# Optimization experiments

Hardware: AMD Instinct MI355X
Metric: run time of the kernel (lower is better)

## Reference

```python
import jax, jax.numpy as jnp
import numpy as np
from jax import lax

TAU = 2.0
V_TH = 1.0
ALPHA = 4.0   # spikingjelly surrogate.Sigmoid default
BN_EPS = 1e-5
HEADS = 8


def lif(x):
    """Multi-step LIF neuron (tau=2, v_reset=0, hard reset, detach_reset).
    x: [T, ...] -> spikes [T, ...]. Forward is Heaviside; sigmoid surrogate
    is wired in via straight-through for the bwd variant."""
    def step(v, xt):
        v = v + (xt - v) / TAU                      # charge
        sg = jax.nn.sigmoid(ALPHA * (v - V_TH))     # surrogate
        hard = (v >= V_TH).astype(x.dtype)
        spike = sg + lax.stop_gradient(hard - sg)   # fwd: hard, bwd: sigmoid'
        v = v * (1.0 - lax.stop_gradient(spike))    # detached hard reset to 0
        return v, spike
    _, s = lax.scan(step, jnp.zeros_like(x[0]), x)
    return s


def conv1x1_bn(x, w, g, b, m, var, bias=None):
    # x: [N, C, H, W]; 1x1 conv == channel matmul, then eval-mode BN
    y = jnp.einsum('nchw,dc->ndhw', x, w)
    if bias is not None:
        y = y + bias[None, :, None, None]
    scale = g / jnp.sqrt(var + BN_EPS)
    shift = b - m * scale
    return y * scale[None, :, None, None] + shift[None, :, None, None]


def to_heads(x, T, B, C, H, W):
    # [T,B,C,H,W] -> [T,B,heads,N,hd]
    N = H * W
    hd = C // HEADS
    x = x.reshape(T, B, C, N).transpose(0, 1, 3, 2)          # [T,B,N,C]
    return x.reshape(T, B, N, HEADS, hd).transpose(0, 1, 3, 2, 4)


def _forward(x, q_w, q_bn_g, q_bn_b, q_bn_m, q_bn_v,
             k_w, k_bn_g, k_bn_b, k_bn_m, k_bn_v,
             v_w, v_bn_g, v_bn_b, v_bn_m, v_bn_v,
             out_w, out_b, out_bn_g, out_bn_b, out_bn_m, out_bn_v):
    T, B, C, H, W = x.shape
    N = H * W
    identity = x

    xs = lif(x)                                  # shortcut_lif
    x_qkv = xs.reshape(T * B, C, H, W)

    q = lif(conv1x1_bn(x_qkv, q_w, q_bn_g, q_bn_b, q_bn_m, q_bn_v).reshape(T, B, C, H, W))
    k = lif(conv1x1_bn(x_qkv, k_w, k_bn_g, k_bn_b, k_bn_m, k_bn_v).reshape(T, B, C, H, W))
    v = lif(conv1x1_bn(x_qkv, v_w, v_bn_g, v_bn_b, v_bn_m, v_bn_v).reshape(T, B, C, H, W))

    qh = to_heads(q, T, B, C, H, W)              # [T,B,h,N,hd]
    kh = to_heads(k, T, B, C, H, W)
    vh = to_heads(v, T, B, C, H, W)

    kv = jnp.sum(kh * vh, axis=-2, keepdims=True)   # [T,B,h,1,hd]
    kv = lif(kv)                                    # talking_heads_proj_lif
    y = qh * kv                                     # [T,B,h,N,hd]

    # [T,B,h,N,hd] -> transpose(3,4) -> [T,B,h,hd,N] -> [T,B,C,H,W]
    y = y.transpose(0, 1, 2, 4, 3).reshape(T, B, C, H, W)
    y = conv1x1_bn(y.reshape(T * B, C, H, W), out_w, out_bn_g, out_bn_b,
                   out_bn_m, out_bn_v, bias=out_b).reshape(T, B, C, H, W)
    return y + identity, vh


def setup_inputs() -> dict:
    key = jax.random.key(0)
    ks = jax.random.split(key, 6)
    T, B, C, H, W = 4, 32, 512, 14, 14
    inp = {
        'x': jax.random.normal(ks[0], (T, B, C, H, W), dtype=jnp.float32),
        'q_w': jax.random.normal(ks[1], (C, C), dtype=jnp.float32) * 0.05,
        'k_w': jax.random.normal(ks[2], (C, C), dtype=jnp.float32) * 0.05,
        'v_w': jax.random.normal(ks[3], (C, C), dtype=jnp.float32) * 0.05,
        'out_w': jax.random.normal(ks[4], (C, C), dtype=jnp.float32) * 0.05,
        'out_b': jnp.zeros((C,), dtype=jnp.float32),
    }
    for p in ('q', 'k', 'v', 'out'):
        inp[f'{p}_bn_g'] = jnp.ones((C,), dtype=jnp.float32)
        inp[f'{p}_bn_b'] = jnp.zeros((C,), dtype=jnp.float32)
        inp[f'{p}_bn_m'] = jnp.zeros((C,), dtype=jnp.float32)
        inp[f'{p}_bn_v'] = jnp.ones((C,), dtype=jnp.float32)
    return inp


def reference(x, q_w, q_bn_g, q_bn_b, q_bn_m, q_bn_v,
              k_w, k_bn_g, k_bn_b, k_bn_m, k_bn_v,
              v_w, v_bn_g, v_bn_b, v_bn_m, v_bn_v,
              out_w, out_b, out_bn_g, out_bn_b, out_bn_m, out_bn_v):
    return _forward(x, q_w, q_bn_g, q_bn_b, q_bn_m, q_bn_v,
                    k_w, k_bn_g, k_bn_b, k_bn_m, k_bn_v,
                    v_w, v_bn_g, v_bn_b, v_bn_m, v_bn_v,
                    out_w, out_b, out_bn_g, out_bn_b, out_bn_m, out_bn_v)
```

## Files before the change

### kernel.cpp

```cpp
#include <hip/hip_runtime.h>
#include <math.h>

#define T_   4
#define B_   32
#define C_   512
#define N_   196
#define TB_  128
#define M_   25088
#define BNP_ 6272
#define OUT1_ 12845056

typedef unsigned short ushort_t;
typedef __attribute__((ext_vector_type(8)))  __bf16 bf16x8;
typedef __attribute__((ext_vector_type(16))) float  f32x16;

__device__ __forceinline__ ushort_t f2bf(float f) {
    unsigned int u = __float_as_uint(f);
    u = u + 0x7FFFu + ((u >> 16) & 1u);
    return (ushort_t)(u >> 16);
}
__device__ __forceinline__ float bf2f(ushort_t h) {
    return __uint_as_float(((unsigned int)h) << 16);
}

#define GL2LDS(gp, lp) \
    __builtin_amdgcn_global_load_lds((const __attribute__((address_space(1))) void*)(gp), \
                                     (__attribute__((address_space(3))) void*)(lp), 16, 0, 0)

__global__ void bn_prep_kernel(
    const float* __restrict__ qg, const float* __restrict__ qb, const float* __restrict__ qm, const float* __restrict__ qv,
    const float* __restrict__ kg, const float* __restrict__ kb, const float* __restrict__ km, const float* __restrict__ kvr,
    const float* __restrict__ vg, const float* __restrict__ vb, const float* __restrict__ vm, const float* __restrict__ vv,
    const float* __restrict__ og, const float* __restrict__ ob, const float* __restrict__ om, const float* __restrict__ ov,
    const float* __restrict__ obias,
    float* __restrict__ scale_qkv, float* __restrict__ shift_qkv,
    float* __restrict__ scale_o,   float* __restrict__ shift_o)
{
    int i = blockIdx.x * 256 + threadIdx.x;
    if (i < 3 * C_) {
        int p = i >> 9, dl = i & 511;
        const float* g = (p == 0) ? qg : (p == 1) ? kg : vg;
        const float* b = (p == 0) ? qb : (p == 1) ? kb : vb;
        const float* m = (p == 0) ? qm : (p == 1) ? km : vm;
        const float* r = (p == 0) ? qv : (p == 1) ? kvr : vv;
        float sc = g[dl] / sqrtf(r[dl] + 1e-5f);
        scale_qkv[i] = sc;
        shift_qkv[i] = b[dl] - m[dl] * sc;
    }
    if (i < C_) {
        float sc = og[i] / sqrtf(ov[i] + 1e-5f);
        scale_o[i] = sc;
        shift_o[i] = ob[i] - om[i] * sc + obias[i] * sc;
    }
}

__global__ void split_kernel(const float* __restrict__ qw, const float* __restrict__ kw,
                             const float* __restrict__ vw, const float* __restrict__ ow,
                             ushort_t* __restrict__ wsplit, ushort_t* __restrict__ osplit)
{
    int i = blockIdx.x * 256 + threadIdx.x;
    int d = i >> 9, c = i & 511;
    const float* src = (d < 512) ? qw : (d < 1024) ? kw : vw;
    float wv = src[(d & 511) * 512 + c];
    ushort_t h = f2bf(wv);
    float r1 = wv - bf2f(h);
    ushort_t mm = f2bf(r1);
    float r2 = r1 - bf2f(mm);
    ushort_t l = f2bf(r2);
    wsplit[((size_t)d * 3 + 0) * 512 + c] = h;
    wsplit[((size_t)d * 3 + 1) * 512 + c] = mm;
    wsplit[((size_t)d * 3 + 2) * 512 + c] = l;
    if (d < 512)
        osplit[(size_t)d * 512 + c] = f2bf(ow[d * 512 + c]);
}

__global__ __launch_bounds__(256)
void lifx_kernel(const float* __restrict__ x, ushort_t* __restrict__ xs)
{
    __shared__ ushort_t tile[64 * 66];
    const int tid = threadIdx.x;
    const int b = blockIdx.z, c0 = blockIdx.y * 64, n0 = blockIdx.x * 64;
    const int j = tid & 63, w = tid >> 6;
    const bool nok = (n0 + j) < N_;
    float v[16];
#pragma unroll
    for (int r = 0; r < 16; ++r) v[r] = 0.f;
    for (int t = 0; t < T_; ++t) {
        const float* xb = x + ((size_t)((t * B_ + b) * C_ + c0)) * N_ + n0 + j;
#pragma unroll
        for (int r = 0; r < 16; ++r) {
            int i = w * 16 + r;
            float xv = nok ? xb[(size_t)i * N_] : 0.f;
            v[r] = v[r] + (xv - v[r]) * 0.5f;
            bool s = (v[r] >= 1.0f);
            tile[j * 66 + i] = s ? 0x3F80 : 0;
            if (s) v[r] = 0.f;
        }
        __syncthreads();
#pragma unroll
        for (int p = 0; p < 2; ++p) {
            int w2 = tid + p * 256;
            int jj = w2 >> 3, ck = w2 & 7;
            if (n0 + jj < N_) {
                const unsigned int* src = reinterpret_cast<const unsigned int*>(&tile[jj * 66 + ck * 8]);
                uint4 dv; dv.x = src[0]; dv.y = src[1]; dv.z = src[2]; dv.w = src[3];
                size_t mp = (size_t)(b * N_ + n0 + jj) * 4 + t;
                *reinterpret_cast<uint4*>(&xs[mp * 512 + c0 + ck * 8]) = dv;
            }
        }
        __syncthreads();
    }
}

__global__ __launch_bounds__(256, 2)
void qkv_gemm_lif(const ushort_t* __restrict__ W, const ushort_t* __restrict__ X,
                  const float* __restrict__ scale, const float* __restrict__ shift,
                  ushort_t* __restrict__ spk, float* __restrict__ out2)
{
    __shared__ ushort_t Xs[16 * 512];
    __shared__ ushort_t Ws[24 * 512];
    const int tid = threadIdx.x, wid = tid >> 6, lane = tid & 63;
    const int m0 = blockIdx.x * 256;
    const int d0 = blockIdx.y * 128;
    const int mw = (wid & 1) * 128, dw = (wid >> 1) * 64;
    const int row32 = lane & 31, khalf = lane >> 5;

    f32x16 acc[4][2] = {};

    for (int k0 = 0; k0 < 512; k0 += 32) {
        __syncthreads();
        for (int q = wid; q < 16; q += 4) {
            int mb = q >> 1, ks = q & 1;
            const ushort_t* g = X + (size_t)(m0 + mb * 32 + row32) * 512 + k0 + ks * 16 + khalf * 8;
            GL2LDS(g, &Xs[q * 512]);
        }
        for (int q = wid; q < 24; q += 4) {
            int s = q >> 3, rem = q & 7, db = rem >> 1, ks = rem & 1;
            const ushort_t* g = W + ((size_t)(d0 + db * 32 + row32) * 3 + s) * 512 + k0 + ks * 16 + khalf * 8;
            GL2LDS(g, &Ws[q * 512]);
        }
        __syncthreads();

#pragma unroll
        for (int ks = 0; ks < 2; ++ks) {
            bf16x8 xfr[4];
#pragma unroll
            for (int i = 0; i < 4; ++i)
                xfr[i] = *reinterpret_cast<const bf16x8*>(&Xs[(((mw >> 5) + i) * 2 + ks) * 512 + lane * 8]);
#pragma unroll
            for (int s = 0; s < 3; ++s)
#pragma unroll
                for (int j = 0; j < 2; ++j) {
                    bf16x8 wfr = *reinterpret_cast<const bf16x8*>(
                        &Ws[(s * 8 + ((dw >> 5) + j) * 2 + ks) * 512 + lane * 8]);
#pragma unroll
                    for (int i = 0; i < 4; ++i)
                        acc[i][j] = __builtin_amdgcn_mfma_f32_32x32x16_bf16(xfr[i], wfr, acc[i][j], 0, 0, 0);
                }
        }
    }

    const int p = d0 >> 9;
    const bool isV = (p == 2);
    ushort_t* plane = spk + (size_t)p * ((size_t)M_ * 512);
#pragma unroll
    for (int j = 0; j < 2; ++j) {
        int d = d0 + dw + j * 32 + row32;
        float sc = scale[d], sh = shift[d];
        int dl = d & 511;
        int h = dl >> 6, hd = dl & 63;
#pragma unroll
        for (int i = 0; i < 4; ++i) {
            int bnb = (m0 + mw + i * 32) >> 2;
            f32x16 a = acc[i][j];
#pragma unroll
            for (int g = 0; g < 4; ++g) {
                int bn = bnb + 2 * g + khalf;
                float p0 = fmaf(a[4 * g + 0], sc, sh);
                float p1 = fmaf(a[4 * g + 1], sc, sh);
                float p2 = fmaf(a[4 * g + 2], sc, sh);
                float p3 = fmaf(a[4 * g + 3], sc, sh);
                float v = p0 * 0.5f;
                bool s0 = (v >= 1.f); if (s0) v = 0.f;
                v = v + (p1 - v) * 0.5f;
                bool s1 = (v >= 1.f); if (s1) v = 0.f;
                v = v + (p2 - v) * 0.5f;
                bool s2 = (v >= 1.f); if (s2) v = 0.f;
                v = v + (p3 - v) * 0.5f;
                bool s3 = (v >= 1.f);
                ushort_t* b0 = plane + (size_t)bn * 512 + dl;
                b0[0]                      = s0 ? 0x3F80 : 0;
                b0[(size_t)BNP_ * 512]     = s1 ? 0x3F80 : 0;
                b0[(size_t)2 * BNP_ * 512] = s2 ? 0x3F80 : 0;
                b0[(size_t)3 * BNP_ * 512] = s3 ? 0x3F80 : 0;
                if (isV) {
                    int b = bn / N_, n = bn - b * N_;
                    float* o = out2 + (((size_t)b * 8 + h) * N_ + n) * 64 + hd;
                    o[0]                       = s0 ? 1.f : 0.f;
                    o[(size_t)1 * (OUT1_ / 4)] = s1 ? 1.f : 0.f;
                    o[(size_t)2 * (OUT1_ / 4)] = s2 ? 1.f : 0.f;
                    o[(size_t)3 * (OUT1_ / 4)] = s3 ? 1.f : 0.f;
                }
            }
        }
    }
}

__global__ void kv_part_kernel(const ushort_t* __restrict__ ks, const ushort_t* __restrict__ vs,
                               float* __restrict__ kvpart)
{
    int tb = blockIdx.x >> 1;
    int c  = (blockIdx.x & 1) * 256 + threadIdx.x;
    const ushort_t* kb = ks + (size_t)tb * N_ * 512 + c;
    const ushort_t* vb = vs + (size_t)tb * N_ * 512 + c;
    int cnt = 0;
    for (int n = 0; n < N_; ++n)
        cnt += (kb[(size_t)n * 512] & vb[(size_t)n * 512]) ? 1 : 0;
    kvpart[tb * 512 + c] = (float)cnt;
}

__global__ void kv_lif_kernel(const float* __restrict__ kvpart, ushort_t* __restrict__ kvs)
{
    int i = blockIdx.x * 256 + threadIdx.x;
    if (i >= B_ * C_) return;
    int b = i >> 9, c = i & 511;
    float v = 0.f;
#pragma unroll
    for (int t = 0; t < T_; ++t) {
        float y = kvpart[((t * B_ + b) << 9) + c];
        v = v + (y - v) * 0.5f;
        bool s = (v >= 1.f);
        kvs[((t * B_ + b) << 9) + c] = s ? 0x3F80 : 0;
        if (s) v = 0.f;
    }
}

__global__ void muly_kernel(const ushort_t* __restrict__ qs, const ushort_t* __restrict__ kvs,
                            ushort_t* __restrict__ y)
{
    int i = blockIdx.x * 256 + threadIdx.x;
    int m = i >> 6, cq = (i & 63) * 8;
    int tb = m / N_;
    uint4 q = *reinterpret_cast<const uint4*>(&qs[(size_t)m * 512 + cq]);
    uint4 k = *reinterpret_cast<const uint4*>(&kvs[(size_t)tb * 512 + cq]);
    uint4 o; o.x = q.x & k.x; o.y = q.y & k.y; o.z = q.z & k.z; o.w = q.w & k.w;
    *reinterpret_cast<uint4*>(&y[(size_t)m * 512 + cq]) = o;
}

__global__ __launch_bounds__(256)
void out_gemm(const ushort_t* __restrict__ A, const ushort_t* __restrict__ Bm,
              const float* __restrict__ scale, const float* __restrict__ shift,
              const float* __restrict__ xid, float* __restrict__ out)
{
    __shared__ ushort_t As[8 * 512];
    __shared__ ushort_t Bs[8 * 512];
    const int tid = threadIdx.x, wid = tid >> 6, lane = tid & 63;
    const int d0 = blockIdx.y * 128, m0 = blockIdx.x * 128;
    const int dw = (wid >> 1) * 64, mw = (wid & 1) * 64;
    const int row32 = lane & 31, khalf = lane >> 5;

    f32x16 acc[2][2] = {};

    for (int k0 = 0; k0 < 512; k0 += 32) {
        __syncthreads();
        for (int q = wid; q < 8; q += 4) {
            int db = q >> 1, ks = q & 1;
            const ushort_t* g = A + (size_t)(d0 + db * 32 + row32) * 512 + k0 + ks * 16 + khalf * 8;
            GL2LDS(g, &As[q * 512]);
        }
        for (int q = wid; q < 8; q += 4) {
            int mb = q >> 1, ks = q & 1;
            const ushort_t* g = Bm + (size_t)(m0 + mb * 32 + row32) * 512 + k0 + ks * 16 + khalf * 8;
            GL2LDS(g, &Bs[q * 512]);
        }
        __syncthreads();

#pragma unroll
        for (int ks = 0; ks < 2; ++ks) {
            bf16x8 afr[2];
#pragma unroll
            for (int i = 0; i < 2; ++i)
                afr[i] = *reinterpret_cast<const bf16x8*>(&As[(((dw >> 5) + i) * 2 + ks) * 512 + lane * 8]);
#pragma unroll
            for (int j = 0; j < 2; ++j) {
                bf16x8 bfr = *reinterpret_cast<const bf16x8*>(&Bs[(((mw >> 5) + j) * 2 + ks) * 512 + lane * 8]);
#pragma unroll
                for (int i = 0; i < 2; ++i)
                    acc[i][j] = __builtin_amdgcn_mfma_f32_32x32x16_bf16(afr[i], bfr, acc[i][j], 0, 0, 0);
            }
        }
    }

#pragma unroll
    for (int j = 0; j < 2; ++j) {
        int m = m0 + mw + j * 32 + row32;
        int tb = m / N_;
        int n  = m - tb * N_;
        size_t mbase = (size_t)tb * (C_ * N_) + n;
#pragma unroll
        for (int i = 0; i < 2; ++i) {
            int dbase = d0 + dw + i * 32 + 4 * khalf;
            f32x16 a = acc[i][j];
#pragma unroll
            for (int g = 0; g < 4; ++g) {
#pragma unroll
                for (int t = 0; t < 4; ++t) {
                    int d = dbase + t + 8 * g;
                    float val = fmaf(a[4 * g + t], scale[d], shift[d]);
                    size_t ad = mbase + (size_t)d * N_;
                    out[ad] = val + xid[ad];
                }
            }
        }
    }
}

extern "C" void kernel_launch(void* const* d_in, const int* in_sizes, int n_in,
                              void* d_out, int out_size, void* d_ws, size_t ws_size,
                              hipStream_t stream)
{
    const float* x    = (const float*)d_in[0];
    const float* q_w  = (const float*)d_in[1];
    const float* k_w  = (const float*)d_in[2];
    const float* v_w  = (const float*)d_in[3];
    const float* o_w  = (const float*)d_in[4];
    const float* o_b  = (const float*)d_in[5];
    const float* qg = (const float*)d_in[6],  *qb = (const float*)d_in[7],
               *qm = (const float*)d_in[8],  *qv = (const float*)d_in[9];
    const float* kg = (const float*)d_in[10], *kb = (const float*)d_in[11],
               *km = (const float*)d_in[12], *kv = (const float*)d_in[13];
    const float* vg = (const float*)d_in[14], *vb = (const float*)d_in[15],
               *vm = (const float*)d_in[16], *vv = (const float*)d_in[17];
    const float* og = (const float*)d_in[18], *ob = (const float*)d_in[19],
               *om = (const float*)d_in[20], *ov = (const float*)d_in[21];

    float* out1  = (float*)d_out;
    float* out2f = out1 + OUT1_;

    ushort_t* spk    = (ushort_t*)d_ws;
    ushort_t* xs     = spk + (size_t)3 * M_ * 512;
    ushort_t* wsplit = xs + (size_t)M_ * 512;
    ushort_t* osplit = wsplit + (size_t)1536 * 3 * 512;
    float*    kvpart = (float*)(osplit + (size_t)512 * 512);
    ushort_t* kvs    = (ushort_t*)(kvpart + TB_ * C_);
    float*    scq    = (float*)(kvs + TB_ * C_);
    float*    shq    = scq + 3 * C_;
    float*    sco    = shq + 3 * C_;
    float*    sho    = sco + C_;

    ushort_t* ksp = spk + (size_t)M_ * 512;
    ushort_t* vsp = spk + (size_t)2 * M_ * 512;

    bn_prep_kernel<<<8, 256, 0, stream>>>(qg, qb, qm, qv, kg, kb, km, kv,
                                          vg, vb, vm, vv, og, ob, om, ov, o_b,
                                          scq, shq, sco, sho);

    split_kernel<<<(1536 * 512) / 256, 256, 0, stream>>>(q_w, k_w, v_w, o_w, wsplit, osplit);

    lifx_kernel<<<dim3(4, 8, 32), 256, 0, stream>>>(x, xs);

    qkv_gemm_lif<<<dim3(98, 12), 256, 0, stream>>>(wsplit, xs, scq, shq, spk, out2f);

    kv_part_kernel<<<256, 256, 0, stream>>>(ksp, vsp, kvpart);

    kv_lif_kernel<<<64, 256, 0, stream>>>(kvpart, kvs);

    muly_kernel<<<(M_ * 64) / 256, 256, 0, stream>>>(spk, kvs, xs );

    out_gemm<<<dim3(196, 4), 256, 0, stream>>>(osplit, xs, sco, sho, x, out1);
}
```

Baseline: 450.8 us.

## Fuse prep kernels, drop third weight split, fuse mask into out GEMM, remap blocks

Merges the BN-prep and weight-split kernels into one launch and cuts the QKV weight split from three bf16 terms to two, reducing MFMA work and weight traffic by a third. The q·kv masking kernel is removed: out_gemm now ANDs q spikes with kv spikes while staging its B tile into LDS, so the intermediate y is never written or re-read. kv_part is split into four row chunks per channel and combined with atomicAdd, with the accumulator zeroed in the prep kernel. Both GEMMs switch to 1D grids with an XCD-aware swizzle for L2 locality. Dropping the third split term lowers precision of the pre-LIF activations, which may flip spikes near threshold.

```diff
diff --git a/kernel.cpp b/kernel.cpp
--- a/kernel.cpp
+++ b/kernel.cpp
@@ -27,16 +27,31 @@
     __builtin_amdgcn_global_load_lds((const __attribute__((address_space(1))) void*)(gp), \
                                      (__attribute__((address_space(3))) void*)(lp), 16, 0, 0)
 
-__global__ void bn_prep_kernel(
+__global__ void prep_kernel(
+    const float* __restrict__ qw, const float* __restrict__ kw,
+    const float* __restrict__ vw, const float* __restrict__ ow,
     const float* __restrict__ qg, const float* __restrict__ qb, const float* __restrict__ qm, const float* __restrict__ qv,
     const float* __restrict__ kg, const float* __restrict__ kb, const float* __restrict__ km, const float* __restrict__ kvr,
     const float* __restrict__ vg, const float* __restrict__ vb, const float* __restrict__ vm, const float* __restrict__ vv,
     const float* __restrict__ og, const float* __restrict__ ob, const float* __restrict__ om, const float* __restrict__ ov,
     const float* __restrict__ obias,
+    ushort_t* __restrict__ wsplit, ushort_t* __restrict__ osplit,
     float* __restrict__ scale_qkv, float* __restrict__ shift_qkv,
-    float* __restrict__ scale_o,   float* __restrict__ shift_o)
+    float* __restrict__ scale_o,   float* __restrict__ shift_o,
+    float* __restrict__ kvpart)
 {
     int i = blockIdx.x * 256 + threadIdx.x;
+    int d = i >> 9, c = i & 511;
+    const float* src = (d < 512) ? qw : (d < 1024) ? kw : vw;
+    float wv = src[(d & 511) * 512 + c];
+    ushort_t h = f2bf(wv);
+    float r1 = wv - bf2f(h);
+    ushort_t mm = f2bf(r1);
+    wsplit[((size_t)d * 2 + 0) * 512 + c] = h;
+    wsplit[((size_t)d * 2 + 1) * 512 + c] = mm;
+    if (d < 512)
+        osplit[(size_t)d * 512 + c] = f2bf(ow[d * 512 + c]);
+
     if (i < 3 * C_) {
         int p = i >> 9, dl = i & 511;
         const float* g = (p == 0) ? qg : (p == 1) ? kg : vg;
@@ -52,26 +67,7 @@
         scale_o[i] = sc;
         shift_o[i] = ob[i] - om[i] * sc + obias[i] * sc;
     }
-}
-
-__global__ void split_kernel(const float* __restrict__ qw, const float* __restrict__ kw,
-                             const float* __restrict__ vw, const float* __restrict__ ow,
-                             ushort_t* __restrict__ wsplit, ushort_t* __restrict__ osplit)
-{
-    int i = blockIdx.x * 256 + threadIdx.x;
-    int d = i >> 9, c = i & 511;
-    const float* src = (d < 512) ? qw : (d < 1024) ? kw : vw;
-    float wv = src[(d & 511) * 512 + c];
-    ushort_t h = f2bf(wv);
-    float r1 = wv - bf2f(h);
-    ushort_t mm = f2bf(r1);
-    float r2 = r1 - bf2f(mm);
-    ushort_t l = f2bf(r2);
-    wsplit[((size_t)d * 3 + 0) * 512 + c] = h;
-    wsplit[((size_t)d * 3 + 1) * 512 + c] = mm;
-    wsplit[((size_t)d * 3 + 2) * 512 + c] = l;
-    if (d < 512)
-        osplit[(size_t)d * 512 + c] = f2bf(ow[d * 512 + c]);
+    if (i < TB_ * C_) kvpart[i] = 0.f;
 }
 
 __global__ __launch_bounds__(256)
@@ -117,11 +113,17 @@
                   const float* __restrict__ scale, const float* __restrict__ shift,
                   ushort_t* __restrict__ spk, float* __restrict__ out2)
 {
+    const int id = blockIdx.x;
+    const int xw = id & 7, local = id >> 3;
+    const int ml = local / 12, d_t = local - ml * 12;
+    const int m_t = ml * 8 + xw;
+    if (m_t >= 98) return;
+    const int m0 = m_t * 256;
+    const int d0 = d_t * 128;
+
     __shared__ ushort_t Xs[16 * 512];
-    __shared__ ushort_t Ws[24 * 512];
+    __shared__ ushort_t Ws[16 * 512];
     const int tid = threadIdx.x, wid = tid >> 6, lane = tid & 63;
-    const int m0 = blockIdx.x * 256;
-    const int d0 = blockIdx.y * 128;
     const int mw = (wid & 1) * 128, dw = (wid >> 1) * 64;
     const int row32 = lane & 31, khalf = lane >> 5;
 
@@ -134,9 +136,9 @@
             const ushort_t* g = X + (size_t)(m0 + mb * 32 + row32) * 512 + k0 + ks * 16 + khalf * 8;
             GL2LDS(g, &Xs[q * 512]);
         }
-        for (int q = wid; q < 24; q += 4) {
+        for (int q = wid; q < 16; q += 4) {
             int s = q >> 3, rem = q & 7, db = rem >> 1, ks = rem & 1;
-            const ushort_t* g = W + ((size_t)(d0 + db * 32 + row32) * 3 + s) * 512 + k0 + ks * 16 + khalf * 8;
+            const ushort_t* g = W + ((size_t)(d0 + db * 32 + row32) * 2 + s) * 512 + k0 + ks * 16 + khalf * 8;
             GL2LDS(g, &Ws[q * 512]);
         }
         __syncthreads();
@@ -148,7 +150,7 @@
             for (int i = 0; i < 4; ++i)
                 xfr[i] = *reinterpret_cast<const bf16x8*>(&Xs[(((mw >> 5) + i) * 2 + ks) * 512 + lane * 8]);
 #pragma unroll
-            for (int s = 0; s < 3; ++s)
+            for (int s = 0; s < 2; ++s)
 #pragma unroll
                 for (int j = 0; j < 2; ++j) {
                     bf16x8 wfr = *reinterpret_cast<const bf16x8*>(
@@ -170,7 +172,7 @@
         int dl = d & 511;
         int h = dl >> 6, hd = dl & 63;
 #pragma unroll
-        for (int i = 0; i < 4; ++i) {
+    for (int i = 0; i < 4; ++i) {
             int bnb = (m0 + mw + i * 32) >> 2;
             f32x16 a = acc[i][j];
 #pragma unroll
@@ -209,14 +211,16 @@
 __global__ void kv_part_kernel(const ushort_t* __restrict__ ks, const ushort_t* __restrict__ vs,
                                float* __restrict__ kvpart)
 {
-    int tb = blockIdx.x >> 1;
-    int c  = (blockIdx.x & 1) * 256 + threadIdx.x;
+    int id = blockIdx.x;
+    int tb = id >> 3, r = id & 7;
+    int c  = (r & 1) * 256 + threadIdx.x;
+    int n0 = (r >> 1) * 49;
     const ushort_t* kb = ks + (size_t)tb * N_ * 512 + c;
     const ushort_t* vb = vs + (size_t)tb * N_ * 512 + c;
     int cnt = 0;
-    for (int n = 0; n < N_; ++n)
+    for (int n = n0; n < n0 + 49; ++n)
         cnt += (kb[(size_t)n * 512] & vb[(size_t)n * 512]) ? 1 : 0;
-    kvpart[tb * 512 + c] = (float)cnt;
+    atomicAdd(&kvpart[tb * 512 + c], (float)cnt);
 }
 
 __global__ void kv_lif_kernel(const float* __restrict__ kvpart, ushort_t* __restrict__ kvs)
@@ -235,29 +239,32 @@
     }
 }
 
-__global__ void muly_kernel(const ushort_t* __restrict__ qs, const ushort_t* __restrict__ kvs,
-                            ushort_t* __restrict__ y)
-{
-    int i = blockIdx.x * 256 + threadIdx.x;
-    int m = i >> 6, cq = (i & 63) * 8;
-    int tb = m / N_;
-    uint4 q = *reinterpret_cast<const uint4*>(&qs[(size_t)m * 512 + cq]);
-    uint4 k = *reinterpret_cast<const uint4*>(&kvs[(size_t)tb * 512 + cq]);
-    uint4 o; o.x = q.x & k.x; o.y = q.y & k.y; o.z = q.z & k.z; o.w = q.w & k.w;
-    *reinterpret_cast<uint4*>(&y[(size_t)m * 512 + cq]) = o;
-}
-
 __global__ __launch_bounds__(256)
-void out_gemm(const ushort_t* __restrict__ A, const ushort_t* __restrict__ Bm,
+void out_gemm(const ushort_t* __restrict__ A, const ushort_t* __restrict__ qs,
+              const ushort_t* __restrict__ kvs,
               const float* __restrict__ scale, const float* __restrict__ shift,
               const float* __restrict__ xid, float* __restrict__ out)
 {
+    const int id = blockIdx.x;
+    const int xw = id & 7, local = id >> 3;
+    const int m_t = (local >> 2) * 8 + xw, d_t = local & 3;
+    if (m_t >= 196) return;
+    const int m0 = m_t * 128, d0 = d_t * 128;
+
     __shared__ ushort_t As[8 * 512];
     __shared__ ushort_t Bs[8 * 512];
     const int tid = threadIdx.x, wid = tid >> 6, lane = tid & 63;
-    const int d0 = blockIdx.y * 128, m0 = blockIdx.x * 128;
     const int dw = (wid >> 1) * 64, mw = (wid & 1) * 64;
     const int row32 = lane & 31, khalf = lane >> 5;
+
+    int sm[2], stb[2], sq[2], sL[2];
+#pragma unroll
+    for (int u = 0; u < 2; ++u) {
+        int s = tid + u * 256;
+        sq[u] = s >> 6; sL[u] = s & 63;
+        sm[u] = m0 + (sq[u] >> 1) * 32 + (sL[u] & 31);
+        stb[u] = sm[u] / N_;
+    }
 
     f32x16 acc[2][2] = {};
 
@@ -268,10 +275,13 @@
             const ushort_t* g = A + (size_t)(d0 + db * 32 + row32) * 512 + k0 + ks * 16 + khalf * 8;
             GL2LDS(g, &As[q * 512]);
         }
-        for (int q = wid; q < 8; q += 4) {
-            int mb = q >> 1, ks = q & 1;
-            const ushort_t* g = Bm + (size_t)(m0 + mb * 32 + row32) * 512 + k0 + ks * 16 + khalf * 8;
-            GL2LDS(g, &Bs[q * 512]);
+#pragma unroll
+        for (int u = 0; u < 2; ++u) {
+            int kk = k0 + (sq[u] & 1) * 16 + (sL[u] >> 5) * 8;
+            uint4 qv = *reinterpret_cast<const uint4*>(&qs[(size_t)sm[u] * 512 + kk]);
+            uint4 kv = *reinterpret_cast<const uint4*>(&kvs[(size_t)stb[u] * 512 + kk]);
+            uint4 o; o.x = qv.x & kv.x; o.y = qv.y & kv.y; o.z = qv.z & kv.z; o.w = qv.w & kv.w;
+            *reinterpret_cast<uint4*>(&Bs[sq[u] * 512 + sL[u] * 8]) = o;
         }
         __syncthreads();
 
@@ -340,7 +350,7 @@
     ushort_t* spk    = (ushort_t*)d_ws;
     ushort_t* xs     = spk + (size_t)3 * M_ * 512;
     ushort_t* wsplit = xs + (size_t)M_ * 512;
-    ushort_t* osplit = wsplit + (size_t)1536 * 3 * 512;
+    ushort_t* osplit = wsplit + (size_t)1536 * 2 * 512;
     float*    kvpart = (float*)(osplit + (size_t)512 * 512);
     ushort_t* kvs    = (ushort_t*)(kvpart + TB_ * C_);
     float*    scq    = (float*)(kvs + TB_ * C_);
@@ -348,24 +358,22 @@
     float*    sco    = shq + 3 * C_;
     float*    sho    = sco + C_;
 
+    ushort_t* qsp = spk;
     ushort_t* ksp = spk + (size_t)M_ * 512;
     ushort_t* vsp = spk + (size_t)2 * M_ * 512;
 
-    bn_prep_kernel<<<8, 256, 0, stream>>>(qg, qb, qm, qv, kg, kb, km, kv,
-                                          vg, vb, vm, vv, og, ob, om, ov, o_b,
-                                          scq, shq, sco, sho);
-
-    split_kernel<<<(1536 * 512) / 256, 256, 0, stream>>>(q_w, k_w, v_w, o_w, wsplit, osplit);
+    prep_kernel<<<(1536 * 512) / 256, 256, 0, stream>>>(
+        q_w, k_w, v_w, o_w,
+        qg, qb, qm, qv, kg, kb, km, kv, vg, vb, vm, vv, og, ob, om, ov, o_b,
+        wsplit, osplit, scq, shq, sco, sho, kvpart);
 
     lifx_kernel<<<dim3(4, 8, 32), 256, 0, stream>>>(x, xs);
 
-    qkv_gemm_lif<<<dim3(98, 12), 256, 0, stream>>>(wsplit, xs, scq, shq, spk, out2f);
-
-    kv_part_kernel<<<256, 256, 0, stream>>>(ksp, vsp, kvpart);
+    qkv_gemm_lif<<<1200, 256, 0, stream>>>(wsplit, xs, scq, shq, spk, out2f);
+
+    kv_part_kernel<<<1024, 256, 0, stream>>>(ksp, vsp, kvpart);
 
     kv_lif_kernel<<<64, 256, 0, stream>>>(kvpart, kvs);
 
-    muly_kernel<<<(M_ * 64) / 256, 256, 0, stream>>>(spk, kvs, xs );
-
-    out_gemm<<<dim3(196, 4), 256, 0, stream>>>(osplit, xs, sco, sho, x, out1);
-}
+    out_gemm<<<800, 256, 0, stream>>>(osplit, qsp, kvs, sco, sho, x, out1);
+}
```

After: 407.4 us. 9.6% less time.
